# Performance work log

Measured on AMD Instinct MI355X. Metric: run time of the kernel, lower is better.

Reference implementation:

```python
import jax, jax.numpy as jnp
import numpy as np

N = 100000   # nodes
E = 1600000  # edges
D = 128      # input_dim == hidden_dim
L = 4        # n_layers
G = 128      # num graphs
NC = 10      # n_classes
EPS = 1e-5


def setup_inputs() -> dict:
    key = jax.random.key(0)
    ks = jax.random.split(key, 12)
    x = jax.random.normal(ks[0], (N, D), jnp.float32)
    edge_index = jax.random.randint(ks[1], (2, E), 0, N, dtype=jnp.int64)
    batch = jnp.sort(jax.random.randint(ks[2], (N,), 0, G, dtype=jnp.int64))
    s = 1.0 / np.sqrt(D)
    conv_w = jax.random.normal(ks[3], (L, D, D), jnp.float32) * s
    conv_b = jnp.zeros((L, D), jnp.float32)
    gn_weight = jnp.ones((L, D), jnp.float32)
    gn_bias = jnp.zeros((L, D), jnp.float32)
    gn_mean_scale = jnp.ones((L, D), jnp.float32)
    dense_w1 = jax.random.normal(ks[4], (D, D), jnp.float32) * s
    dense_b1 = jnp.zeros((D,), jnp.float32)
    bn_gamma = jnp.ones((D,), jnp.float32)
    bn_beta = jnp.zeros((D,), jnp.float32)
    bn_mean = jnp.zeros((D,), jnp.float32)   # running stats (eval mode)
    bn_var = jnp.ones((D,), jnp.float32)
    dense_w2 = jax.random.normal(ks[5], (D, NC), jnp.float32) * s
    dense_b2 = jnp.zeros((NC,), jnp.float32)
    return dict(x=x, edge_index=edge_index, batch=batch, conv_w=conv_w,
                conv_b=conv_b, gn_weight=gn_weight, gn_bias=gn_bias,
                gn_mean_scale=gn_mean_scale, dense_w1=dense_w1, dense_b1=dense_b1,
                bn_gamma=bn_gamma, bn_beta=bn_beta, bn_mean=bn_mean, bn_var=bn_var,
                dense_w2=dense_w2, dense_b2=dense_b2)


def _graph_norm(x, batch, counts, weight, bias, mean_scale):
    # PyG GraphNorm: (x - alpha*mean) / sqrt(var + eps) * weight + bias, per graph
    mean = jax.ops.segment_sum(x, batch, num_segments=G) / counts        # [G, D]
    sub = x - mean_scale * mean[batch]                                    # [N, D]
    var = jax.ops.segment_sum(sub * sub, batch, num_segments=G) / counts  # [G, D]
    return weight * sub * jax.lax.rsqrt(var + EPS)[batch] + bias


def reference(x, edge_index, batch, conv_w, conv_b, gn_weight, gn_bias,
              gn_mean_scale, dense_w1, dense_b1, bn_gamma, bn_beta,
              bn_mean, bn_var, dense_w2, dense_b2):
    # GCNConv normalization with self-loops (symmetric D^-1/2 (A+I) D^-1/2)
    loop = jnp.arange(N, dtype=edge_index.dtype)
    src = jnp.concatenate([edge_index[0], loop])
    dst = jnp.concatenate([edge_index[1], loop])
    deg = jax.ops.segment_sum(jnp.ones((E + N,), x.dtype), dst, num_segments=N)
    dis = jax.lax.rsqrt(deg)  # deg >= 1 due to self-loops
    nrm = (dis[src] * dis[dst])[:, None]                                  # [E+N, 1]
    counts = jax.ops.segment_sum(jnp.ones((N, 1), x.dtype), batch, num_segments=G)

    x_res = x  # input_dim == hidden_dim -> no input projection
    for i in range(L):
        h = x @ conv_w[i]                                # [N, D]
        h = jax.ops.segment_sum(h[src] * nrm, dst, num_segments=N) + conv_b[i]
        h = _graph_norm(h, batch, counts, gn_weight[i], gn_bias[i], gn_mean_scale[i])
        h = jax.nn.elu(h)
        # dropout: identity in eval mode
        x = h + x_res
        x_res = x

    pooled = jax.ops.segment_sum(x, batch, num_segments=G)  # global_add_pool [G, D]
    z = pooled @ dense_w1 + dense_b1
    z = bn_gamma * (z - bn_mean) * jax.lax.rsqrt(bn_var + EPS) + bn_beta
    z = jax.nn.relu(z)
    z = z @ dense_w2 + dense_b2
    return (x, z)
```

## Files before the change

### kernel.cpp

```cpp
#include <hip/hip_runtime.h>
#include <stdint.h>

#define N_NODES 100000
#define N_PAD   100032
#define N_EDGES 1600000
#define DIM 128
#define NLAYERS 4
#define NGRAPH 128
#define NCLS 10
#define EPSV 1e-5f
#define NSLOT 32

#define BIN_SHIFT 9
#define NBUCKET ((N_NODES + 511) >> 9)
#define P1_EPB 4096
#define P1_BLOCKS ((N_EDGES + P1_EPB - 1) / P1_EPB)

typedef __attribute__((ext_vector_type(8))) short short8_t;
typedef __attribute__((ext_vector_type(4))) float float4_t;


__device__ __forceinline__ float bf_lo(uint32_t u) { return __uint_as_float(u << 16); }
__device__ __forceinline__ float bf_hi(uint32_t u) { return __uint_as_float(u & 0xffff0000u); }
__device__ __forceinline__ uint32_t f2bf_rne(float f) {
    uint32_t x = __float_as_uint(f);
    return (x + 0x7fffu + ((x >> 16) & 1u)) >> 16;
}
__device__ __forceinline__ uint32_t pack_bf2(float a, float b) {
    return f2bf_rne(a) | (f2bf_rne(b) << 16);
}
__device__ __forceinline__ float4 unpack4(uint2 u) {
    return make_float4(bf_lo(u.x), bf_hi(u.x), bf_lo(u.y), bf_hi(u.y));
}
__device__ __forceinline__ float ub0(uint32_t u) { return (float)( u        & 0xffu); }
__device__ __forceinline__ float ub1(uint32_t u) { return (float)((u >>  8) & 0xffu); }
__device__ __forceinline__ float ub2(uint32_t u) { return (float)((u >> 16) & 0xffu); }
__device__ __forceinline__ float ub3(uint32_t u) { return (float)( u >> 24        ); }
__device__ __forceinline__ float elu_neg(float x) { return __expf(x) - 1.f; }


__global__ void k_node_meta(const int* __restrict__ batch, int* __restrict__ gstart,
                            int* __restrict__ bcnt) {
    int i = blockIdx.x * blockDim.x + threadIdx.x;
    if (i < NBUCKET) bcnt[i] = 0;
    if (i >= N_NODES) return;
    int b = batch[i];
    if (i == 0) {
        for (int g = 0; g <= b; g++) gstart[g] = 0;
    } else {
        int bp = batch[i - 1];
        for (int g = bp + 1; g <= b; g++) gstart[g] = i;
    }
    if (i == N_NODES - 1) {
        for (int g = b + 1; g <= NGRAPH; g++) gstart[g] = N_NODES;
    }
}

__global__ __launch_bounds__(256) void k_bhist(const int* __restrict__ ei, int* __restrict__ bcnt) {
    __shared__ int hist[NBUCKET];
    int t = threadIdx.x;
    for (int i = t; i < NBUCKET; i += 256) hist[i] = 0;
    __syncthreads();
    int e0 = blockIdx.x * P1_EPB;
    int e1 = e0 + P1_EPB; if (e1 > N_EDGES) e1 = N_EDGES;
    for (int e = e0 + t; e < e1; e += 256) atomicAdd(&hist[ei[N_EDGES + e] >> BIN_SHIFT], 1);
    __syncthreads();
    for (int i = t; i < NBUCKET; i += 256) if (hist[i]) atomicAdd(&bcnt[i], hist[i]);
}

__global__ __launch_bounds__(256) void k_bscan(const int* __restrict__ bcnt,
                                               int* __restrict__ bucket_off, int* __restrict__ bcur) {
    __shared__ int s[256];
    int t = threadIdx.x;
    int v = (t < NBUCKET) ? bcnt[t] : 0;
    s[t] = v; __syncthreads();
    for (int off = 1; off < 256; off <<= 1) {
        int a = (t >= off) ? s[t - off] : 0;
        __syncthreads();
        s[t] += a;
        __syncthreads();
    }
    if (t < NBUCKET) { bucket_off[t] = s[t] - v; bcur[t] = s[t] - v; }
    if (t == 0) bucket_off[NBUCKET] = s[255];
}

__global__ __launch_bounds__(256) void k_bin_edges(const int* __restrict__ ei,
                                                   int* __restrict__ bcur,
                                                   int2* __restrict__ binned) {
    __shared__ int hist[NBUCKET];
    __shared__ int base[NBUCKET];
    int t = threadIdx.x;
    int e0 = blockIdx.x * P1_EPB;
    int e1 = e0 + P1_EPB; if (e1 > N_EDGES) e1 = N_EDGES;
    for (int i = t; i < NBUCKET; i += 256) hist[i] = 0;
    __syncthreads();
    int myrank[P1_EPB / 256];
    int cnt = 0;
    for (int e = e0 + t; e < e1; e += 256) {
        int d = ei[N_EDGES + e];
        myrank[cnt++] = atomicAdd(&hist[d >> BIN_SHIFT], 1);
    }
    __syncthreads();
    for (int i = t; i < NBUCKET; i += 256) base[i] = atomicAdd(&bcur[i], hist[i]);
    __syncthreads();
    cnt = 0;
    for (int e = e0 + t; e < e1; e += 256) {
        int s = ei[e];
        int d = ei[N_EDGES + e];
        binned[base[d >> BIN_SHIFT] + myrank[cnt++]] = make_int2(s, d);
    }
}

__global__ __launch_bounds__(256) void k_bucket_build(const int2* __restrict__ binned,
                                                      const int* __restrict__ bucket_off,
                                                      int* __restrict__ rowoff,
                                                      float* __restrict__ dis,
                                                      int* __restrict__ psrc) {
    __shared__ int cnt[512];
    __shared__ int sa[512];
    __shared__ int sb[512];
    int b = blockIdx.x;
    int t = threadIdx.x;
    int n0 = b << BIN_SHIFT;
    int j0 = bucket_off[b], j1 = bucket_off[b + 1];
    cnt[t] = 0; cnt[t + 256] = 0;
    __syncthreads();
    for (int j = j0 + t; j < j1; j += 256) atomicAdd(&cnt[binned[j].y & 511], 1);
    __syncthreads();
    sa[t] = cnt[t]; sa[t + 256] = cnt[t + 256];
    __syncthreads();
    int* A = sa; int* B = sb;
    for (int off = 1; off < 512; off <<= 1) {
        int i0 = t, i1 = t + 256;
        B[i0] = A[i0] + ((i0 >= off) ? A[i0 - off] : 0);
        B[i1] = A[i1] + ((i1 >= off) ? A[i1 - off] : 0);
        __syncthreads();
        int* tmp = A; A = B; B = tmp;
    }
    for (int i = t; i < 512; i += 256) {
        int n = n0 + i;
        if (n < N_NODES) {
            rowoff[n] = j0 + A[i] - cnt[i];
            dis[n] = rsqrtf((float)(1 + cnt[i]));
        }
    }
    if (b == NBUCKET - 1 && t == 0) rowoff[N_NODES] = N_EDGES;
    for (int idx = t; idx < 512 * NSLOT; idx += 256) {
        int i = idx >> 5, k = idx & (NSLOT - 1);
        int n = n0 + i;
        if (n < N_NODES && k >= cnt[i]) psrc[(size_t)n * NSLOT + k] = (k == cnt[i]) ? n : N_NODES;
    }
}

__global__ __launch_bounds__(256) void k_scatter(const int2* __restrict__ binned,
                                                 const float* __restrict__ dis,
                                                 const int* __restrict__ rowoff,
                                                 const int* __restrict__ bucket_off,
                                                 int2* __restrict__ csc,
                                                 int* __restrict__ psrc) {
    __shared__ int lcur[512];
    int b = blockIdx.x;
    int t = threadIdx.x;
    lcur[t] = 0; lcur[t + 256] = 0;
    __syncthreads();
    int j0 = bucket_off[b], j1 = bucket_off[b + 1];
    for (int j = j0 + t; j < j1; j += 256) {
        int2 sd = binned[j];
        float w = dis[sd.x] * dis[sd.y];
        int rank = atomicAdd(&lcur[sd.y & 511], 1);
        csc[rowoff[sd.y] + rank] = make_int2(sd.x, __float_as_int(w));
        if (rank < NSLOT) psrc[(size_t)sd.y * NSLOT + rank] = sd.x;
    }
}

__global__ void k_cast_w(const float* __restrict__ W, uint32_t* __restrict__ Wt) {
    int i = blockIdx.x * blockDim.x + threadIdx.x;
    if (i >= NLAYERS * DIM * 64) return;
    int l = i / (DIM * 64);
    int n = (i / 64) % DIM;
    int ku = i % 64;
    const float* Wl = W + (size_t)l * DIM * DIM;
    float w0 = Wl[(2 * ku) * DIM + n];
    float w1 = Wl[(2 * ku + 1) * DIM + n];
    Wt[i] = pack_bf2(w0, w1);
}


__device__ __forceinline__ void gemm_phase(const uint32_t (*atile)[68], const uint32_t* __restrict__ Wt,
                                           uint8_t (*ctile8)[132], float* rmaxl,
                                           uint8_t* __restrict__ H8,
                                           float* __restrict__ hsd, const float* __restrict__ dis,
                                           int blk, int t) {
    int wid = t >> 6;
    int lane = t & 63;
    int quad = lane >> 4;
    int s15 = lane & 15;

    float4_t acc[8];
#pragma unroll
    for (int i = 0; i < 8; i++) acc[i] = (float4_t){0.f, 0.f, 0.f, 0.f};

#pragma unroll
    for (int kk = 0; kk < 4; kk++) {
        uint4 au = *(const uint4*)&atile[wid * 16 + s15][quad * 4 + kk * 16];
        short8_t a = __builtin_bit_cast(short8_t, au);
#pragma unroll
        for (int nt = 0; nt < 8; nt++) {
            uint4 bu = *(const uint4*)(Wt + (size_t)(nt * 16 + s15) * 64 + kk * 16 + quad * 4);
            short8_t b = __builtin_bit_cast(short8_t, bu);
            acc[nt] = __builtin_amdgcn_mfma_f32_16x16x32_bf16(a, b, acc[nt], 0, 0, 0);
        }
    }
    __syncthreads();

    float sinv[4];
#pragma unroll
    for (int r = 0; r < 4; r++) {
        float m = fabsf(acc[0][r]);
#pragma unroll
        for (int nt = 1; nt < 8; nt++) m = fmaxf(m, fabsf(acc[nt][r]));
        m = fmaxf(m, __shfl_xor(m, 1));
        m = fmaxf(m, __shfl_xor(m, 2));
        m = fmaxf(m, __shfl_xor(m, 4));
        m = fmaxf(m, __shfl_xor(m, 8));
        if (s15 == 0) rmaxl[wid * 16 + quad * 4 + r] = m;
        sinv[r] = (m > 0.f) ? 127.f / m : 0.f;
    }
#pragma unroll
    for (int nt = 0; nt < 8; nt++) {
#pragma unroll
        for (int r = 0; r < 4; r++) {
            int qv = (int)fmaf(acc[nt][r], sinv[r], 128.5f);
            ctile8[wid * 16 + quad * 4 + r][nt * 16 + s15] = (uint8_t)qv;
        }
    }
    __syncthreads();
    uint8_t* Hb = H8 + (size_t)blk * 64 * 128;
    float* Hsb = hsd + (size_t)blk * 64;
#pragma unroll
    for (int i = 0; i < 8; i++) {
        int idx = t + 256 * i;
        int row = idx >> 5, cu = idx & 31;
        uint32_t v = *(const uint32_t*)&ctile8[row][cu * 4];
        ((uint32_t*)Hb)[(size_t)row * 32 + cu] = v;
        if (cu == 0) {
            size_t gr = (size_t)blk * 64 + row;
            float dv = (gr < N_NODES) ? dis[gr] : 0.f;
            Hsb[row] = rmaxl[row] * (1.f / 127.f) * dv;
        }
    }
}

#define GEMM_SMEM \
    __shared__ __align__(16) char smem[64 * 68 * 4]; \
    uint32_t (*atile)[68] = (uint32_t(*)[68])smem; \
    uint8_t (*ctile8)[132] = (uint8_t(*)[132])smem; \
    float* rmaxl = (float*)(smem + 64 * 132);

__global__ __launch_bounds__(256) void k_gemm0(const float* __restrict__ X, const uint32_t* __restrict__ Wt,
                                               uint8_t* __restrict__ H8, float* __restrict__ hsd,
                                               const float* __restrict__ dis) {
    GEMM_SMEM
    int t = threadIdx.x;
    size_t row0 = (size_t)blockIdx.x * 64;
#pragma unroll
    for (int i = 0; i < 8; i++) {
        int idx = t + 256 * i;
        int row = idx >> 5, q = idx & 31;
        size_t gr = row0 + row;
        uint2 p = make_uint2(0u, 0u);
        if (gr < N_NODES) {
            float4 v = ((const float4*)(X + gr * DIM))[q];
            p.x = pack_bf2(v.x, v.y);
            p.y = pack_bf2(v.z, v.w);
        }
        *(uint2*)&atile[row][q * 2] = p;
    }
    __syncthreads();
    gemm_phase(atile, Wt, ctile8, rmaxl, H8, hsd, dis, blockIdx.x, t);
}

template <bool RBF>
__global__ __launch_bounds__(256) void k_norm_gemm(const uint32_t* __restrict__ A, const int* __restrict__ batch,
                                                   const float* __restrict__ amean, const float* __restrict__ rstd,
                                                   const float* __restrict__ gw, const float* __restrict__ gb,
                                                   const void* __restrict__ res, uint32_t* __restrict__ res_out,
                                                   const uint32_t* __restrict__ Wt,
                                                   uint8_t* __restrict__ H8, float* __restrict__ hsd,
                                                   const float* __restrict__ dis) {
    GEMM_SMEM
    int t = threadIdx.x;
    size_t row0 = (size_t)blockIdx.x * 64;
#pragma unroll
    for (int i = 0; i < 8; i++) {
        int idx = t + 256 * i;
        int row = idx >> 5, q = idx & 31;
        size_t gr = row0 + row;
        uint2 p = make_uint2(0u, 0u);
        if (gr < N_NODES) {
            int g = batch[gr];
            float4 v = unpack4(((const uint2*)(A + gr * 64))[q]);
            float4 am = ((const float4*)amean)[g * 32 + q];
            float4 rs = ((const float4*)rstd)[g * 32 + q];
            float4 w = ((const float4*)gw)[q];
            float4 b = ((const float4*)gb)[q];
            float4 r;
            if (RBF) r = unpack4(((const uint2*)((const uint32_t*)res + gr * 64))[q]);
            else     r = ((const float4*)res)[gr * 32 + q];
            float4 o;
            o.x = w.x * (v.x - am.x) * rs.x + b.x;
            o.y = w.y * (v.y - am.y) * rs.y + b.y;
            o.z = w.z * (v.z - am.z) * rs.z + b.z;
            o.w = w.w * (v.w - am.w) * rs.w + b.w;
            o.x = ((o.x > 0.f) ? o.x : elu_neg(o.x)) + r.x;
            o.y = ((o.y > 0.f) ? o.y : elu_neg(o.y)) + r.y;
            o.z = ((o.z > 0.f) ? o.z : elu_neg(o.z)) + r.z;
            o.w = ((o.w > 0.f) ? o.w : elu_neg(o.w)) + r.w;
            p.x = pack_bf2(o.x, o.y);
            p.y = pack_bf2(o.z, o.w);
            ((uint2*)(res_out + gr * 64))[q] = p;
        }
        *(uint2*)&atile[row][q * 2] = p;
    }
    __syncthreads();
    gemm_phase(atile, Wt, ctile8, rmaxl, H8, hsd, dis, blockIdx.x, t);
}


#define ACC8(WS, U) \
    acc[0] += WS * ub0(U.x); acc[1] += WS * ub1(U.x); \
    acc[2] += WS * ub2(U.x); acc[3] += WS * ub3(U.x); \
    acc[4] += WS * ub0(U.y); acc[5] += WS * ub1(U.y); \
    acc[6] += WS * ub2(U.y); acc[7] += WS * ub3(U.y);

__global__ __launch_bounds__(256, 4) void k_aggregate(const uint8_t* __restrict__ H8,
                                                      const float* __restrict__ hsd,
                                                      const int* __restrict__ psrc,
                                                      const int2* __restrict__ csc,
                                                      const int* __restrict__ rowoff,
                                                      const float* __restrict__ dis,
                                                      const float* __restrict__ bias,
                                                      uint32_t* __restrict__ Out) {
    int wid = threadIdx.x >> 6;
    int lane = threadIdx.x & 63;
    uint32_t hq = (uint32_t)((lane >> 4) & 1);
    uint32_t s  = (uint32_t)(lane & 15);
    uint32_t n  = (uint32_t)blockIdx.x * 8u + ((uint32_t)wid << 1) + (uint32_t)(lane >> 5);
    uint32_t s8 = s << 3;

    float dd = dis[n];
    int b0 = rowoff[n], b1 = rowoff[n + 1];
    const int4* P = (const int4*)(psrc + ((size_t)n << 5) + (hq << 4));
    int4 pa = P[0], pb = P[1], pc = P[2], pd = P[3];

    float h0 = hsd[(uint32_t)pa.x], h1 = hsd[(uint32_t)pa.y];
    float h2 = hsd[(uint32_t)pa.z], h3 = hsd[(uint32_t)pa.w];
    float h4 = hsd[(uint32_t)pb.x], h5 = hsd[(uint32_t)pb.y];
    float h6 = hsd[(uint32_t)pb.z], h7 = hsd[(uint32_t)pb.w];
    uint2 u0 = *(const uint2*)(H8 + (((uint32_t)pa.x << 7) | s8));
    uint2 u1 = *(const uint2*)(H8 + (((uint32_t)pa.y << 7) | s8));
    uint2 u2 = *(const uint2*)(H8 + (((uint32_t)pa.z << 7) | s8));
    uint2 u3 = *(const uint2*)(H8 + (((uint32_t)pa.w << 7) | s8));
    uint2 u4 = *(const uint2*)(H8 + (((uint32_t)pb.x << 7) | s8));
    uint2 u5 = *(const uint2*)(H8 + (((uint32_t)pb.y << 7) | s8));
    uint2 u6 = *(const uint2*)(H8 + (((uint32_t)pb.z << 7) | s8));
    uint2 u7 = *(const uint2*)(H8 + (((uint32_t)pb.w << 7) | s8));

    float acc[8];
#pragma unroll
    for (int k = 0; k < 8; k++) acc[k] = 0.f;

    ACC8(h0, u0); ACC8(h1, u1); ACC8(h2, u2); ACC8(h3, u3);
    ACC8(h4, u4); ACC8(h5, u5); ACC8(h6, u6); ACC8(h7, u7);

    float h8  = hsd[(uint32_t)pc.x], h9  = hsd[(uint32_t)pc.y];
    float h10 = hsd[(uint32_t)pc.z], h11 = hsd[(uint32_t)pc.w];
    float h12 = hsd[(uint32_t)pd.x], h13 = hsd[(uint32_t)pd.y];
    float h14 = hsd[(uint32_t)pd.z], h15 = hsd[(uint32_t)pd.w];
    uint2 u8  = *(const uint2*)(H8 + (((uint32_t)pc.x << 7) | s8));
    uint2 u9  = *(const uint2*)(H8 + (((uint32_t)pc.y << 7) | s8));
    uint2 u10 = *(const uint2*)(H8 + (((uint32_t)pc.z << 7) | s8));
    uint2 u11 = *(const uint2*)(H8 + (((uint32_t)pc.w << 7) | s8));
    uint2 u12 = *(const uint2*)(H8 + (((uint32_t)pd.x << 7) | s8));
    uint2 u13 = *(const uint2*)(H8 + (((uint32_t)pd.y << 7) | s8));
    uint2 u14 = *(const uint2*)(H8 + (((uint32_t)pd.z << 7) | s8));
    uint2 u15 = *(const uint2*)(H8 + (((uint32_t)pd.w << 7) | s8));

    ACC8(h8, u8);  ACC8(h9, u9);  ACC8(h10, u10); ACC8(h11, u11);
    ACC8(h12, u12); ACC8(h13, u13); ACC8(h14, u14); ACC8(h15, u15);

    float offs = ((h0 + h1) + (h2 + h3)) + ((h4 + h5) + (h6 + h7))
               + ((h8 + h9) + (h10 + h11)) + ((h12 + h13) + (h14 + h15));

    if (b1 - b0 >= NSLOT) {
        float wsf = (hq == 0) ? hsd[n] : 0.f;
        uint2 uu = *(const uint2*)(H8 + ((n << 7) | s8));
        ACC8(wsf, uu);
        offs += wsf;
        for (int j = b0 + NSLOT + (int)hq; j < b1; j += 2) {
            uint32_t sx = (uint32_t)csc[j].x;
            float w = hsd[sx];
            uint2 u = *(const uint2*)(H8 + ((sx << 7) | s8));
            ACC8(w, u);
            offs += w;
        }
    }

#pragma unroll
    for (int k = 0; k < 8; k++) acc[k] += __shfl_xor(acc[k], 16);
    offs += __shfl_xor(offs, 16);

    float corr = -128.f * offs;
    float a0 = hq ? acc[4] : acc[0];
    float a1 = hq ? acc[5] : acc[1];
    float a2 = hq ? acc[6] : acc[2];
    float a3 = hq ? acc[7] : acc[3];
    float4 bb = ((const float4*)bias)[(s << 1) | hq];
    uint2 ov;
    ov.x = pack_bf2(fmaf(dd, a0 + corr, bb.x), fmaf(dd, a1 + corr, bb.y));
    ov.y = pack_bf2(fmaf(dd, a2 + corr, bb.z), fmaf(dd, a3 + corr, bb.w));
    *(uint2*)(Out + ((n << 6) | (s << 2) | (hq << 1))) = ov;
}

__global__ __launch_bounds__(512) void k_stats(const uint32_t* __restrict__ A, const int* __restrict__ gstart,
                                               const float* __restrict__ mscale,
                                               float* __restrict__ amean, float* __restrict__ rstd) {
    __shared__ float L1[8][DIM];
    __shared__ float L2[8][DIM];
    int g = blockIdx.x;
    int t = threadIdx.x;
    int f2 = t & 63;
    int p = t >> 6;
    int s0 = gstart[g], s1 = gstart[g + 1];
    float sa = 0.f, sb = 0.f, qa = 0.f, qb = 0.f;
    for (int n = s0 + p; n < s1; n += 8) {
        uint32_t u = A[(size_t)n * 64 + f2];
        float a = bf_lo(u), b = bf_hi(u);
        sa += a; qa += a * a;
        sb += b; qb += b * b;
    }
    L1[p][2 * f2] = sa; L1[p][2 * f2 + 1] = sb;
    L2[p][2 * f2] = qa; L2[p][2 * f2 + 1] = qb;
    __syncthreads();
    if (t < DIM) {
        float s = 0.f, s2 = 0.f;
#pragma unroll
        for (int i = 0; i < 8; i++) { s += L1[i][t]; s2 += L2[i][t]; }
        int cnt = s1 - s0;
        float inv = (cnt > 0) ? 1.0f / (float)cnt : 0.f;
        float m = s * inv;
        float a = mscale[t];
        float var = s2 * inv - (2.f * a - a * a) * m * m;
        amean[g * DIM + t] = a * m;
        rstd[g * DIM + t] = rsqrtf(var + EPSV);
    }
}

__global__ __launch_bounds__(512) void k_pool_head(const uint32_t* __restrict__ A,
                                                   const uint32_t* __restrict__ resb,
                                                   const int* __restrict__ gstart,
                                                   const float* __restrict__ amean, const float* __restrict__ rstd,
                                                   const float* __restrict__ gw, const float* __restrict__ gb,
                                                   const float* __restrict__ w1, const float* __restrict__ b1,
                                                   const float* __restrict__ gamma, const float* __restrict__ beta,
                                                   const float* __restrict__ rmean, const float* __restrict__ rvar,
                                                   const float* __restrict__ w2, const float* __restrict__ b2,
                                                   float* __restrict__ outx, float* __restrict__ zout) {
    __shared__ float L[8][DIM];
    __shared__ float sp[DIM];
    __shared__ float sz[DIM];
    int g = blockIdx.x, t = threadIdx.x;
    int f2 = t & 63;
    int p = t >> 6;
    int s0 = gstart[g], s1 = gstart[g + 1];
    float am0 = amean[g * DIM + 2 * f2], am1 = amean[g * DIM + 2 * f2 + 1];
    float rs0 = rstd[g * DIM + 2 * f2],  rs1 = rstd[g * DIM + 2 * f2 + 1];
    float w0_ = gw[2 * f2], w1_ = gw[2 * f2 + 1];
    float b0_ = gb[2 * f2], b1_ = gb[2 * f2 + 1];
    float p0 = 0.f, p1 = 0.f;
    for (int n = s0 + p; n < s1; n += 8) {
        uint32_t u = A[(size_t)n * 64 + f2];
        uint32_t ur = resb[(size_t)n * 64 + f2];
        float a = bf_lo(u), b = bf_hi(u);
        float r0 = bf_lo(ur), r1 = bf_hi(ur);
        float o0 = w0_ * (a - am0) * rs0 + b0_;
        float o1 = w1_ * (b - am1) * rs1 + b1_;
        o0 = ((o0 > 0.f) ? o0 : elu_neg(o0)) + r0;
        o1 = ((o1 > 0.f) ? o1 : elu_neg(o1)) + r1;
        ((float2*)(outx + (size_t)n * DIM))[f2] = make_float2(o0, o1);
        p0 += o0; p1 += o1;
    }
    L[p][2 * f2] = p0; L[p][2 * f2 + 1] = p1;
    __syncthreads();
    if (t < DIM) {
        float s = 0.f;
#pragma unroll
        for (int i = 0; i < 8; i++) s += L[i][t];
        sp[t] = s;
    }
    __syncthreads();
    if (t < DIM) {
        float acc = b1[t];
#pragma unroll 8
        for (int k = 0; k < DIM; k++) acc += sp[k] * w1[k * DIM + t];
        acc = gamma[t] * (acc - rmean[t]) * rsqrtf(rvar[t] + EPSV) + beta[t];
        sz[t] = fmaxf(acc, 0.f);
    }
    __syncthreads();
    if (t < NCLS) {
        float a2 = b2[t];
#pragma unroll 8
        for (int k = 0; k < DIM; k++) a2 += sz[k] * w2[k * NCLS + t];
        zout[g * NCLS + t] = a2;
    }
}


extern "C" void kernel_launch(void* const* d_in, const int* in_sizes, int n_in,
                              void* d_out, int out_size, void* d_ws, size_t ws_size,
                              hipStream_t stream) {
    const float* x_in   = (const float*)d_in[0];
    const int*   ei     = (const int*)d_in[1];
    const int*   batch  = (const int*)d_in[2];
    const float* conv_w = (const float*)d_in[3];
    const float* conv_b = (const float*)d_in[4];
    const float* gn_w   = (const float*)d_in[5];
    const float* gn_b   = (const float*)d_in[6];
    const float* gn_ms  = (const float*)d_in[7];
    const float* w1     = (const float*)d_in[8];
    const float* b1     = (const float*)d_in[9];
    const float* bng    = (const float*)d_in[10];
    const float* bnb    = (const float*)d_in[11];
    const float* bnm    = (const float*)d_in[12];
    const float* bnv    = (const float*)d_in[13];
    const float* w2     = (const float*)d_in[14];
    const float* b2     = (const float*)d_in[15];

    float* out_x = (float*)d_out;
    float* out_z = out_x + (size_t)N_NODES * DIM;

    char* ws = (char*)d_ws;
    size_t off = 0;
    auto alloc = [&](size_t bytes) -> void* {
        void* p = ws + off;
        off += (bytes + 255) / 256 * 256;
        return p;
    };
    uint8_t* h8      = (uint8_t*)alloc(sizeof(uint8_t) * (size_t)N_PAD * 128);
    float*   hsd     = (float*)alloc(sizeof(float) * (size_t)N_PAD);
    uint32_t* agg    = (uint32_t*)alloc(sizeof(uint32_t) * (size_t)N_NODES * 64);
    uint32_t* resb   = (uint32_t*)alloc(sizeof(uint32_t) * (size_t)N_NODES * 64);
    int2*  csc       = (int2*)alloc(sizeof(int2) * (size_t)N_EDGES);
    int2*  binned    = (int2*)alloc(sizeof(int2) * (size_t)N_EDGES);
    int*   psrc      = (int*)alloc(sizeof(int) * (size_t)N_NODES * NSLOT);
    uint32_t* wt     = (uint32_t*)alloc(sizeof(uint32_t) * NLAYERS * DIM * 64);
    float* dis       = (float*)alloc(sizeof(float) * N_NODES);
    int*   rowoff    = (int*)alloc(sizeof(int) * (N_NODES + 1));
    int*   bcnt      = (int*)alloc(sizeof(int) * NBUCKET);
    int*   boffb     = (int*)alloc(sizeof(int) * (NBUCKET + 1));
    int*   bcur      = (int*)alloc(sizeof(int) * NBUCKET);
    int*   gstart    = (int*)alloc(sizeof(int) * (NGRAPH + 1));
    float* amean     = (float*)alloc(sizeof(float) * NGRAPH * DIM);
    float* rstd      = (float*)alloc(sizeof(float) * NGRAPH * DIM);

    k_node_meta<<<(N_NODES + 255) / 256, 256, 0, stream>>>(batch, gstart, bcnt);
    k_bhist<<<P1_BLOCKS, 256, 0, stream>>>(ei, bcnt);
    k_bscan<<<1, 256, 0, stream>>>(bcnt, boffb, bcur);
    k_bin_edges<<<P1_BLOCKS, 256, 0, stream>>>(ei, bcur, binned);
    k_bucket_build<<<NBUCKET, 256, 0, stream>>>(binned, boffb, rowoff, dis, psrc);
    k_scatter<<<NBUCKET, 256, 0, stream>>>(binned, dis, rowoff, boffb, csc, psrc);
    k_cast_w<<<(NLAYERS * DIM * 64 + 255) / 256, 256, 0, stream>>>(conv_w, wt);

    k_gemm0<<<N_PAD / 64, 256, 0, stream>>>(x_in, wt, h8, hsd, dis);
    for (int l = 0; l < NLAYERS; l++) {
        k_aggregate<<<N_NODES / 8, 256, 0, stream>>>(h8, hsd, psrc, csc, rowoff, dis,
                                                     conv_b + (size_t)l * DIM, agg);
        k_stats<<<NGRAPH, 512, 0, stream>>>(agg, gstart, gn_ms + (size_t)l * DIM, amean, rstd);
        if (l == 0) {
            k_norm_gemm<false><<<N_PAD / 64, 256, 0, stream>>>(agg, batch, amean, rstd, gn_w, gn_b,
                                                               (const void*)x_in, resb,
                                                               wt + (size_t)1 * DIM * 64, h8, hsd, dis);
        } else if (l < NLAYERS - 1) {
            k_norm_gemm<true><<<N_PAD / 64, 256, 0, stream>>>(agg, batch, amean, rstd,
                                                              gn_w + (size_t)l * DIM, gn_b + (size_t)l * DIM,
                                                              (const void*)resb, resb,
                                                              wt + (size_t)(l + 1) * DIM * 64, h8, hsd, dis);
        } else {
            k_pool_head<<<NGRAPH, 512, 0, stream>>>(agg, resb, gstart, amean, rstd,
                                                    gn_w + (size_t)l * DIM, gn_b + (size_t)l * DIM,
                                                    w1, b1, bng, bnb, bnm, bnv, w2, b2, out_x, out_z);
        }
    }
}
```

Measured before the change: 737.8 us.

## Split final norm-pool across eight blocks per graph with atomic pooling

The final layer's normalize/ELU/residual/pool kernel previously ran one 512-thread block per graph (128 blocks), which leaves most of the GPU idle. It now launches eight blocks per graph, each covering an interleaved slice of nodes, and accumulates per-graph sums into a zeroed global buffer with atomicAdd. The dense head moves into a separate small kernel. This costs an extra launch, zero-initialisation in the meta kernel, and makes the float summation order nondeterministic.

```diff
diff --git a/kernel.cpp b/kernel.cpp
--- a/kernel.cpp
+++ b/kernel.cpp
@@ -10,6 +10,7 @@
 #define NCLS 10
 #define EPSV 1e-5f
 #define NSLOT 32
+#define POOL_PARTS 8
 
 #define BIN_SHIFT 9
 #define NBUCKET ((N_NODES + 511) >> 9)
@@ -40,9 +41,10 @@
 
 
 __global__ void k_node_meta(const int* __restrict__ batch, int* __restrict__ gstart,
-                            int* __restrict__ bcnt) {
+                            int* __restrict__ bcnt, float* __restrict__ pooled) {
     int i = blockIdx.x * blockDim.x + threadIdx.x;
     if (i < NBUCKET) bcnt[i] = 0;
+    if (i < NGRAPH * DIM) pooled[i] = 0.f;
     if (i >= N_NODES) return;
     int b = batch[i];
     if (i == 0) {
@@ -456,29 +458,26 @@
     }
 }
 
-__global__ __launch_bounds__(512) void k_pool_head(const uint32_t* __restrict__ A,
+__global__ __launch_bounds__(512) void k_norm_pool(const uint32_t* __restrict__ A,
                                                    const uint32_t* __restrict__ resb,
                                                    const int* __restrict__ gstart,
                                                    const float* __restrict__ amean, const float* __restrict__ rstd,
                                                    const float* __restrict__ gw, const float* __restrict__ gb,
-                                                   const float* __restrict__ w1, const float* __restrict__ b1,
-                                                   const float* __restrict__ gamma, const float* __restrict__ beta,
-                                                   const float* __restrict__ rmean, const float* __restrict__ rvar,
-                                                   const float* __restrict__ w2, const float* __restrict__ b2,
-                                                   float* __restrict__ outx, float* __restrict__ zout) {
+                                                   float* __restrict__ outx, float* __restrict__ pooled) {
     __shared__ float L[8][DIM];
-    __shared__ float sp[DIM];
-    __shared__ float sz[DIM];
-    int g = blockIdx.x, t = threadIdx.x;
+    int g = blockIdx.x >> 3;
+    int part = blockIdx.x & 7;
+    int t = threadIdx.x;
     int f2 = t & 63;
     int p = t >> 6;
+    int slice = part * 8 + p;
     int s0 = gstart[g], s1 = gstart[g + 1];
     float am0 = amean[g * DIM + 2 * f2], am1 = amean[g * DIM + 2 * f2 + 1];
     float rs0 = rstd[g * DIM + 2 * f2],  rs1 = rstd[g * DIM + 2 * f2 + 1];
     float w0_ = gw[2 * f2], w1_ = gw[2 * f2 + 1];
     float b0_ = gb[2 * f2], b1_ = gb[2 * f2 + 1];
     float p0 = 0.f, p1 = 0.f;
-    for (int n = s0 + p; n < s1; n += 8) {
+    for (int n = s0 + slice; n < s1; n += 64) {
         uint32_t u = A[(size_t)n * 64 + f2];
         uint32_t ur = resb[(size_t)n * 64 + f2];
         float a = bf_lo(u), b = bf_hi(u);
@@ -496,16 +495,24 @@
         float s = 0.f;
 #pragma unroll
         for (int i = 0; i < 8; i++) s += L[i][t];
-        sp[t] = s;
-    }
-    __syncthreads();
-    if (t < DIM) {
-        float acc = b1[t];
+        if (s != 0.f) atomicAdd(&pooled[g * DIM + t], s);
+    }
+}
+
+__global__ __launch_bounds__(128) void k_head(const float* __restrict__ pooled,
+                                              const float* __restrict__ w1, const float* __restrict__ b1,
+                                              const float* __restrict__ gamma, const float* __restrict__ beta,
+                                              const float* __restrict__ rmean, const float* __restrict__ rvar,
+                                              const float* __restrict__ w2, const float* __restrict__ b2,
+                                              float* __restrict__ zout) {
+    __shared__ float sz[DIM];
+    int g = blockIdx.x, t = threadIdx.x;
+    const float* sp = pooled + g * DIM;
+    float acc = b1[t];
 #pragma unroll 8
-        for (int k = 0; k < DIM; k++) acc += sp[k] * w1[k * DIM + t];
-        acc = gamma[t] * (acc - rmean[t]) * rsqrtf(rvar[t] + EPSV) + beta[t];
-        sz[t] = fmaxf(acc, 0.f);
-    }
+    for (int k = 0; k < DIM; k++) acc += sp[k] * w1[k * DIM + t];
+    acc = gamma[t] * (acc - rmean[t]) * rsqrtf(rvar[t] + EPSV) + beta[t];
+    sz[t] = fmaxf(acc, 0.f);
     __syncthreads();
     if (t < NCLS) {
         float a2 = b2[t];
@@ -562,8 +569,9 @@
     int*   gstart    = (int*)alloc(sizeof(int) * (NGRAPH + 1));
     float* amean     = (float*)alloc(sizeof(float) * NGRAPH * DIM);
     float* rstd      = (float*)alloc(sizeof(float) * NGRAPH * DIM);
-
-    k_node_meta<<<(N_NODES + 255) / 256, 256, 0, stream>>>(batch, gstart, bcnt);
+    float* pooled    = (float*)alloc(sizeof(float) * NGRAPH * DIM);
+
+    k_node_meta<<<(N_NODES + 255) / 256, 256, 0, stream>>>(batch, gstart, bcnt, pooled);
     k_bhist<<<P1_BLOCKS, 256, 0, stream>>>(ei, bcnt);
     k_bscan<<<1, 256, 0, stream>>>(bcnt, boffb, bcur);
     k_bin_edges<<<P1_BLOCKS, 256, 0, stream>>>(ei, bcur, binned);
@@ -586,9 +594,10 @@
                                                               (const void*)resb, resb,
                                                               wt + (size_t)(l + 1) * DIM * 64, h8, hsd, dis);
         } else {
-            k_pool_head<<<NGRAPH, 512, 0, stream>>>(agg, resb, gstart, amean, rstd,
-                                                    gn_w + (size_t)l * DIM, gn_b + (size_t)l * DIM,
-                                                    w1, b1, bng, bnb, bnm, bnv, w2, b2, out_x, out_z);
-        }
-    }
-}
+            k_norm_pool<<<NGRAPH * POOL_PARTS, 512, 0, stream>>>(agg, resb, gstart, amean, rstd,
+                                                                 gn_w + (size_t)l * DIM, gn_b + (size_t)l * DIM,
+                                                                 out_x, pooled);
+            k_head<<<NGRAPH, 128, 0, stream>>>(pooled, w1, b1, bng, bnb, bnm, bnv, w2, b2, out_z);
+        }
+    }
+}
```

After: 724.3 us. Within noise of the previous version (-1.8%).
